# Optimization experiments

Hardware: AMD Instinct MI355X
Metric: run time of the kernel (lower is better)

The kernel has to match this reference:

```python
import jax, jax.numpy as jnp
import numpy as np

D_MODEL, D_STATE, D_CONV, EXPAND = 1024, 16, 4, 2
D_INNER = EXPAND * D_MODEL
B, L = 2, 2048


def setup_inputs() -> dict:
    key = jax.random.key(0)
    ks = jax.random.split(key, 8)
    s = lambda fan: 1.0 / np.sqrt(fan)
    x = jax.random.normal(ks[0], (B, L, D_MODEL), dtype=jnp.float32)
    W_in = jax.random.normal(ks[1], (2 * D_INNER, D_MODEL), dtype=jnp.float32) * s(D_MODEL)
    conv_w = jax.random.normal(ks[2], (D_INNER, 1, D_CONV), dtype=jnp.float32) * s(D_CONV)
    conv_b = jax.random.normal(ks[3], (D_INNER,), dtype=jnp.float32) * 0.01
    A_log = jnp.log(jnp.abs(jax.random.normal(ks[4], (D_INNER, D_STATE), dtype=jnp.float32)) + 1e-4)
    Dp = jnp.ones((D_INNER,), dtype=jnp.float32)
    W_dt = jax.random.normal(ks[5], (D_INNER, D_INNER), dtype=jnp.float32) * s(D_INNER)
    b_dt = jax.random.normal(ks[6], (D_INNER,), dtype=jnp.float32) * 0.01
    W_out = jax.random.normal(ks[7], (D_MODEL, D_INNER), dtype=jnp.float32) * s(D_INNER)
    return {"x": x, "W_in": W_in, "conv_w": conv_w, "conv_b": conv_b,
            "A_log": A_log, "Dp": Dp, "W_dt": W_dt, "b_dt": b_dt, "W_out": W_out}


def _mamba_fwd(x, W_in, conv_w, conv_b, A_log, Dp, W_dt, b_dt, W_out):
    Bsz, Ln, _ = x.shape
    xz = x @ W_in.T                                  # [B, L, 2*d_inner]
    x_proj, z = jnp.split(xz, 2, axis=-1)            # each [B, L, d_inner]
    # depthwise causal conv1d: left-pad d_conv-1 (matches torch pad + [:L] slice)
    xc = jnp.transpose(x_proj, (0, 2, 1))            # [B, C, L]
    xc = jax.lax.conv_general_dilated(
        xc, conv_w, window_strides=(1,), padding=[(D_CONV - 1, 0)],
        dimension_numbers=("NCH", "OIH", "NCH"), feature_group_count=D_INNER)
    xc = xc + conv_b[None, :, None]
    x_act = jax.nn.silu(jnp.transpose(xc, (0, 2, 1)))  # [B, L, d_inner]
    dt = jax.nn.softplus(x_act @ W_dt.T + b_dt)        # [B, L, d_inner]
    A = -jnp.exp(A_log)                                # [d_inner, d_state]

    def step(h, inp):
        xt, dt_t = inp                                 # [B, d_inner] each
        dA = jnp.exp(dt_t[:, :, None] * A[None])       # [B, d_inner, d_state]
        dB = (dt_t * xt)[:, :, None]                   # broadcast over states
        h = dA * h + dB
        y_t = h.sum(axis=-1) + Dp * xt                 # [B, d_inner]
        return h, y_t

    h0 = jnp.zeros((Bsz, D_INNER, D_STATE), dtype=x.dtype)
    xs = (jnp.transpose(x_act, (1, 0, 2)), jnp.transpose(dt, (1, 0, 2)))  # [L, B, d_inner]
    _, ys = jax.lax.scan(step, h0, xs)
    y_ssm = jnp.transpose(ys, (1, 0, 2))               # [B, L, d_inner]
    y_gated = y_ssm * jax.nn.silu(z)
    return y_gated @ W_out.T                           # [B, L, d_model]


def reference(x, W_in, conv_w, conv_b, A_log, Dp, W_dt, b_dt, W_out):
    return _mamba_fwd(x, W_in, conv_w, conv_b, A_log, Dp, W_dt, b_dt, W_out)
```

## Files before the change

### kernel.cpp

```cpp
#include <hip/hip_runtime.h>

#define DMODEL 1024
#define DSTATE 16
#define DCONV  4
#define DINNER 2048
#define BSZ    2
#define LSEQ   2048
#define MTOT   (BSZ * LSEQ)
#define NCH    64
#define LC     (LSEQ / NCH)
#define LOG2E  1.44269504088896f

typedef unsigned short u16;
typedef __attribute__((ext_vector_type(8))) short short8;
typedef __attribute__((ext_vector_type(8))) unsigned short u16x8;
typedef __attribute__((ext_vector_type(4))) float f32x4;

__device__ __forceinline__ float silu_f(float v) {
  return v * __builtin_amdgcn_rcpf(1.f + __builtin_amdgcn_exp2f(-v * LOG2E));
}

__device__ __forceinline__ u16 f2bf(float f) {
  unsigned int u = __float_as_uint(f);
  u += 0x7FFF + ((u >> 16) & 1);
  return (u16)(u >> 16);
}
__device__ __forceinline__ float bf2f(u16 b) { return __uint_as_float(((unsigned int)b) << 16); }

__device__ __forceinline__ void gload_lds16(const u16* g, u16* l) {
  __builtin_amdgcn_global_load_lds((const __attribute__((address_space(1))) unsigned int*)g,
                                   (__attribute__((address_space(3))) unsigned int*)l, 16, 0, 0);
}

__global__ __launch_bounds__(256)
void cast4(const float4* __restrict__ s0, ushort4* __restrict__ d0, int n0,
           const float4* __restrict__ s1, ushort4* __restrict__ d1, int n1,
           const float4* __restrict__ s2, ushort4* __restrict__ d2, int n2,
           const float4* __restrict__ s3, ushort4* __restrict__ d3, int n3) {
  int i = blockIdx.x * 256 + threadIdx.x;
  const float4* s; ushort4* d;
  if (i < n0)                { s = s0; d = d0; }
  else if ((i -= n0) < n1)   { s = s1; d = d1; }
  else if ((i -= n1) < n2)   { s = s2; d = d2; }
  else if ((i -= n2) < n3)   { s = s3; d = d3; }
  else return;
  float4 v = s[i];
  ushort4 o = { f2bf(v.x), f2bf(v.y), f2bf(v.z), f2bf(v.w) };
  d[i] = o;
}

template<int BN, int MODE, int OBF>
__global__ __launch_bounds__(512, 2)
void gemm8p(const u16* __restrict__ A, const u16* __restrict__ Bm,
            const float* __restrict__ bias, void* __restrict__ Cv,
            int M, int N, int K) {
  constexpr int BT  = BN / 32;
  constexpr int TJP = 2;
  constexpr int NPH = BT / TJP;
  constexpr int NBH = BN / 128;
  extern __shared__ __align__(16) u16 smem[];
  u16* As = smem;
  u16* Bs = smem + 2 * 256 * 64;

  const int tid  = threadIdx.x;
  const int lane = tid & 63;
  const int w    = tid >> 6;
  const int quad = lane >> 4;
  const int l16  = lane & 15;
  const int wm   = (w >> 1) * 64;
  const int wn   = (w & 1) * (BN / 2);

  const int nbn = N / BN, nbm = M >> 8;
  const int pid = blockIdx.x;
  const int npg = 4 * nbn;
  const int fm  = (pid / npg) * 4;
  const int gsz = (nbm - fm < 4) ? (nbm - fm) : 4;
  const int bm  = (fm + (pid % gsz)) << 8;
  const int bn  = ((pid % npg) / gsz) * BN;

  const int rseg = lane >> 3;
  const int cd8  = (((lane & 7) ^ rseg) << 3);
  const u16* gA = A  + (size_t)(bm + 16 * w + rseg) * K + cd8;
  const u16* gB = Bm + (size_t)(bn + 16 * w + rseg) * K + cd8;
  u16* lA = &As[(2 * w) << 9];
  u16* lB = &Bs[(2 * w) << 9];
  const int Kmask = K - 1;

  auto stA = [&](int slot, int h, int kt) {
    const size_t go = (size_t)h * 128 * K + ((kt << 6) & Kmask);
    gload_lds16(gA + go,         lA + slot * 16384 + h * 8192);
    gload_lds16(gA + go + 8 * K, lA + slot * 16384 + h * 8192 + 512);
  };
  auto stB = [&](int slot, int h, int kt) {
    const size_t go = (size_t)h * 128 * K + ((kt << 6) & Kmask);
    gload_lds16(gB + go,         lB + slot * (BN * 64) + h * 8192);
    gload_lds16(gB + go + 8 * K, lB + slot * (BN * 64) + h * 8192 + 512);
  };

  int aoff[4][2], boff[BT][2];
#pragma unroll
  for (int t = 0; t < 4; ++t) {
    const int ra = wm + 16 * t + l16;
#pragma unroll
    for (int ks = 0; ks < 2; ++ks)
      aoff[t][ks] = ra * 64 + (((quad + 4 * ks) ^ (ra & 7)) << 3);
  }
#pragma unroll
  for (int tj = 0; tj < BT; ++tj) {
    const int rb = wn + 16 * tj + l16;
#pragma unroll
    for (int ks = 0; ks < 2; ++ks)
      boff[tj][ks] = rb * 64 + (((quad + 4 * ks) ^ (rb & 7)) << 3);
  }

  f32x4 acc[4][BT] = {};
  short8 af[4][2];

#define RD_AF(slot)                                                          \
  { _Pragma("unroll") for (int t = 0; t < 4; ++t)                            \
      _Pragma("unroll") for (int ks = 0; ks < 2; ++ks)                       \
        af[t][ks] = *(const short8*)&As[(slot) * 16384 + aoff[t][ks]]; }

#define VM4 asm volatile("s_waitcnt vmcnt(4)" ::: "memory")
#define NOWAIT ((void)0)

#define PHASE(slot, j, STG, WAIT)                                            \
  {                                                                          \
    if ((j) == 0) RD_AF(slot);                                               \
    short8 bfp[TJP][2];                                                      \
    _Pragma("unroll") for (int jj = 0; jj < TJP; ++jj)                       \
      _Pragma("unroll") for (int ks = 0; ks < 2; ++ks)                       \
        bfp[jj][ks] = *(const short8*)&Bs[(slot) * (BN * 64) +               \
                                          boff[(j) * TJP + jj][ks]];         \
    STG;                                                                     \
    __builtin_amdgcn_s_setprio(1);                                           \
    _Pragma("unroll") for (int ks = 0; ks < 2; ++ks)                         \
      _Pragma("unroll") for (int jj = 0; jj < TJP; ++jj)                     \
        _Pragma("unroll") for (int t = 0; t < 4; ++t)                        \
          acc[t][(j) * TJP + jj] = __builtin_amdgcn_mfma_f32_16x16x32_bf16(  \
              af[t][ks], bfp[jj][ks], acc[t][(j) * TJP + jj], 0, 0, 0);      \
    __builtin_amdgcn_s_setprio(0);                                           \
    asm volatile("s_waitcnt lgkmcnt(0)" ::: "memory");                       \
    WAIT;                                                                    \
    __builtin_amdgcn_s_barrier();                                            \
  }

  stA(0, 0, 0); stA(0, 1, 0);
  stB(0, 0, 0); if (NBH == 2) stB(0, 1, 0);
  stA(1, 0, 1); stA(1, 1, 1);
  VM4;
  __builtin_amdgcn_s_barrier();

  const int niter = K >> 7;
  for (int i = 0; i < niter; ++i) {
    const int tb1 = 2 * i + 1, t2 = 2 * i + 2, t3 = 2 * i + 3;
    if constexpr (NPH == 4) {
      PHASE(0, 0, { stB(1, 0, tb1); },               NOWAIT);
      PHASE(0, 1, { stB(1, 1, tb1); stA(0, 0, t2); }, NOWAIT);
      PHASE(0, 2, { stA(0, 1, t2); },                NOWAIT);
      PHASE(0, 3, {},                                VM4);
      PHASE(1, 0, { stB(0, 0, t2); },                NOWAIT);
      PHASE(1, 1, { stB(0, 1, t2); stA(1, 0, t3); }, NOWAIT);
      PHASE(1, 2, { stA(1, 1, t3); },                NOWAIT);
      PHASE(1, 3, {},                                VM4);
    } else {
      PHASE(0, 0, { stB(1, 0, tb1); },                NOWAIT);
      PHASE(0, 1, { stA(0, 0, t2); stA(0, 1, t2); },  VM4);
      PHASE(1, 0, { stB(0, 0, t2); },                 NOWAIT);
      PHASE(1, 1, { stA(1, 0, t3); stA(1, 1, t3); },  VM4);
    }
  }
#undef PHASE
#undef RD_AF
#undef VM4
#undef NOWAIT

  asm volatile("s_waitcnt vmcnt(0)" ::: "memory");

#pragma unroll
  for (int t = 0; t < 4; ++t) {
    const int row0 = bm + wm + 16 * t + quad * 4;
#pragma unroll
    for (int tj = 0; tj < BT; ++tj) {
      const int col = bn + wn + 16 * tj + l16;
      const float bv = (MODE == 1) ? bias[col] : 0.f;
#pragma unroll
      for (int i2 = 0; i2 < 4; ++i2) {
        float v = acc[t][tj][i2] + bv;
        if (MODE == 1) v = (v > 20.f) ? v : __logf(1.f + __expf(v));
        if (OBF) ((u16*)Cv)[(size_t)(row0 + i2) * N + col] = f2bf(v);
        else     ((float*)Cv)[(size_t)(row0 + i2) * N + col] = v;
      }
    }
  }
}

template<int MODE, int OBF, int BN>
__global__ __launch_bounds__(256)
void hgemm_bk128(const u16* __restrict__ A, const u16* __restrict__ B,
                 const float* __restrict__ bias, void* __restrict__ Cv,
                 int M, int N, int K) {
  constexpr int ASEG = 32;
  constexpr int BSEG = BN / 4;
  constexpr int SPW  = (ASEG + BSEG) / 4;
  constexpr int BT   = BN / 32;
  __shared__ u16 As[128 * 128];
  __shared__ u16 Bs[BN * 128];
  const int tid  = threadIdx.x;
  const int lane = tid & 63;
  const int w    = tid >> 6;
  const int quad = lane >> 4;
  const int l16  = lane & 15;

  const int nbn = N / BN, nbm = M >> 7;
  const int pid = blockIdx.x;
  const int npg = 4 * nbn;
  const int fm  = (pid / npg) * 4;
  const int gsz = (nbm - fm < 4) ? (nbm - fm) : 4;
  const int bm  = (fm + (pid % gsz)) << 7;
  const int bn  = ((pid % npg) / gsz) * BN;

  const int wm = (w & 1) * 64;
  const int wn = (w >> 1) * (BN / 2);

  const int rs4 = lane >> 4;
  const u16* Gp[SPW]; u16* Lp[SPW];
#pragma unroll
  for (int q = 0; q < SPW; ++q) {
    const int g = w * SPW + q;
    if (g < ASEG) {
      const int r  = g * 4 + rs4;
      const int cdk = (lane & 15) ^ (r & 15);
      Gp[q] = A + (size_t)(bm + r) * K + (cdk << 3);
      Lp[q] = &As[g << 9];
    } else {
      const int r  = (g - ASEG) * 4 + rs4;
      const int cdk = (lane & 15) ^ (r & 15);
      Gp[q] = B + (size_t)(bn + r) * K + (cdk << 3);
      Lp[q] = &Bs[(g - ASEG) << 9];
    }
  }

  const short8* Afp[4][4];
  const short8* Bfp[BT][4];
#pragma unroll
  for (int t = 0; t < 4; ++t) {
    const int ra = wm + 16 * t + l16;
#pragma unroll
    for (int ks = 0; ks < 4; ++ks)
      Afp[t][ks] = (const short8*)&As[ra * 128 + (((quad + 4 * ks) ^ (ra & 15)) << 3)];
  }
#pragma unroll
  for (int t = 0; t < BT; ++t) {
    const int rb = wn + 16 * t + l16;
#pragma unroll
    for (int ks = 0; ks < 4; ++ks)
      Bfp[t][ks] = (const short8*)&Bs[rb * 128 + (((quad + 4 * ks) ^ (rb & 15)) << 3)];
  }

  f32x4 acc[4][BT] = {};

  for (int k0 = 0; k0 < K; k0 += 128) {
#pragma unroll
    for (int q = 0; q < SPW; ++q) { gload_lds16(Gp[q], Lp[q]); Gp[q] += 128; }
    __syncthreads();
#pragma unroll
    for (int ks = 0; ks < 4; ++ks) {
      short8 af[4], bf[BT];
#pragma unroll
      for (int t = 0; t < 4; ++t) af[t] = *Afp[t][ks];
#pragma unroll
      for (int t = 0; t < BT; ++t) bf[t] = *Bfp[t][ks];
#pragma unroll
      for (int ti = 0; ti < 4; ++ti)
#pragma unroll
        for (int tj = 0; tj < BT; ++tj)
          acc[ti][tj] = __builtin_amdgcn_mfma_f32_16x16x32_bf16(af[ti], bf[tj],
                                                                acc[ti][tj], 0, 0, 0);
    }
    __syncthreads();
  }

#pragma unroll
  for (int ti = 0; ti < 4; ++ti) {
    const int row0 = bm + wm + 16 * ti + quad * 4;
#pragma unroll
    for (int tj = 0; tj < BT; ++tj) {
      const int col = bn + wn + 16 * tj + l16;
      const float bv = (MODE == 1) ? bias[col] : 0.f;
#pragma unroll
      for (int i = 0; i < 4; ++i) {
        float v = acc[ti][tj][i] + bv;
        if (MODE == 1) v = (v > 20.f) ? v : __logf(1.f + __expf(v));
        if (OBF) ((u16*)Cv)[(size_t)(row0 + i) * N + col] = f2bf(v);
        else     ((float*)Cv)[(size_t)(row0 + i) * N + col] = v;
      }
    }
  }
}

__global__ __launch_bounds__(256)
void conv_silu(const u16* __restrict__ xz, const float* __restrict__ conv_w,
               const float* __restrict__ conv_b, u16* __restrict__ xact) {
  const int i = blockIdx.x * 256 + threadIdx.x;
  const int ko = i & 255;
  const int t  = (i >> 8) & (LSEQ - 1);
  const int b  = i >> 19;
  const int c  = ko << 3;
  float a[8];
  float4 w[8];
#pragma unroll
  for (int j = 0; j < 8; ++j) {
    a[j] = conv_b[c + j];
    w[j] = *(const float4*)(conv_w + (c + j) * DCONV);
  }
#pragma unroll
  for (int k = 0; k < DCONV; ++k) {
    const int tt = t + k - (DCONV - 1);
    if (tt >= 0) {
      const u16x8 v = *(const u16x8*)(xz + ((size_t)(b * LSEQ + tt) << 12) + c);
#pragma unroll
      for (int j = 0; j < 8; ++j)
        a[j] = fmaf(bf2f(v[j]), ((const float*)&w[j])[k], a[j]);
    }
  }
  u16x8 o;
#pragma unroll
  for (int j = 0; j < 8; ++j) o[j] = f2bf(silu_f(a[j]));
  *(u16x8*)(xact + ((size_t)(b * LSEQ + t) << 11) + c) = o;
}


__global__ __launch_bounds__(256, 2)
void scan_pass1(const u16* __restrict__ dtb, const u16* __restrict__ xact,
                const float* __restrict__ A_log,
                u16* __restrict__ hbuf, float* __restrict__ sumdt) {
  const int gid = blockIdx.x * 256 + threadIdx.x;
  const int c  = gid & (DINNER - 1);
  const int ch = (gid >> 11) & (NCH - 1);
  const int b  = gid >> 17;
  float a2[16];
#pragma unroll
  for (int s = 0; s < 16; ++s)
    a2[s] = -__expf(A_log[c * DSTATE + s]) * LOG2E;
  const size_t base = ((size_t)(b * LSEQ + ch * LC) << 11) + c;
  float h[16] = {};
  float sd = 0.f;
  for (int j = 0; j < LC; j += 2) {
    const float dt0 = bf2f(dtb [base + ((size_t)j << 11)]);
    const float xv0 = bf2f(xact[base + ((size_t)j << 11)]);
    const float dt1 = bf2f(dtb [base + ((size_t)(j + 1) << 11)]);
    const float xv1 = bf2f(xact[base + ((size_t)(j + 1) << 11)]);
    const float dx0 = dt0 * xv0, dx1 = dt1 * xv1;
    sd += dt0 + dt1;
#pragma unroll
    for (int s = 0; s < 16; ++s)
      h[s] = fmaf(__builtin_amdgcn_exp2f(dt0 * a2[s]), h[s], dx0);
#pragma unroll
    for (int s = 0; s < 16; ++s)
      h[s] = fmaf(__builtin_amdgcn_exp2f(dt1 * a2[s]), h[s], dx1);
  }
  u16x8* ho = (u16x8*)&hbuf[(((size_t)(b * NCH + ch) * DINNER) + c) << 4];
  u16x8 lo, hi;
#pragma unroll
  for (int s = 0; s < 8; ++s) { lo[s] = f2bf(h[s]); hi[s] = f2bf(h[8 + s]); }
  ho[0] = lo; ho[1] = hi;
  sumdt[(size_t)(b * NCH + ch) * DINNER + c] = sd;
}

__global__ __launch_bounds__(256)
void scan_combine(u16* __restrict__ hbuf, const float* __restrict__ sumdt,
                  const float* __restrict__ A_log) {
  const int gid = blockIdx.x * 256 + threadIdx.x;
  const int s = gid & 15;
  const int c = (gid >> 4) & (DINNER - 1);
  const int b = gid >> 15;
  const float a2 = -__expf(A_log[c * DSTATE + s]) * LOG2E;
  float h = 0.f;
  for (int k = 0; k < NCH; ++k) {
    const size_t o = (((size_t)(b * NCH + k) * DINNER) + c) * 16 + s;
    const float he = bf2f(hbuf[o]);
    const float sd = sumdt[(size_t)(b * NCH + k) * DINNER + c];
    hbuf[o] = f2bf(h);
    h = fmaf(__builtin_amdgcn_exp2f(sd * a2), h, he);
  }
}

__global__ __launch_bounds__(256, 2)
void scan_pass3(const u16* __restrict__ dtb, const u16* __restrict__ xact,
                const u16* __restrict__ xz, const float* __restrict__ A_log,
                const float* __restrict__ Dp, const u16* __restrict__ hbuf,
                u16* __restrict__ yg) {
  const int gid = blockIdx.x * 256 + threadIdx.x;
  const int c  = gid & (DINNER - 1);
  const int ch = (gid >> 11) & (NCH - 1);
  const int b  = gid >> 17;
  float a2[16];
#pragma unroll
  for (int s = 0; s < 16; ++s)
    a2[s] = -__expf(A_log[c * DSTATE + s]) * LOG2E;
  const float dp = Dp[c];
  float h[16];
  const u16x8* hi = (const u16x8*)&hbuf[(((size_t)(b * NCH + ch) * DINNER) + c) << 4];
  const u16x8 vlo = hi[0], vhi = hi[1];
#pragma unroll
  for (int s = 0; s < 8; ++s) { h[s] = bf2f(vlo[s]); h[8 + s] = bf2f(vhi[s]); }
  const size_t base  = ((size_t)(b * LSEQ + ch * LC) << 11) + c;
  const size_t zbase = ((size_t)(b * LSEQ + ch * LC) << 12) + DINNER + c;
  for (int j = 0; j < LC; j += 2) {
    const float dt0 = bf2f(dtb [base + ((size_t)j << 11)]);
    const float xv0 = bf2f(xact[base + ((size_t)j << 11)]);
    const float zv0 = bf2f(xz[zbase + ((size_t)j << 12)]);
    const float dt1 = bf2f(dtb [base + ((size_t)(j + 1) << 11)]);
    const float xv1 = bf2f(xact[base + ((size_t)(j + 1) << 11)]);
    const float zv1 = bf2f(xz[zbase + ((size_t)(j + 1) << 12)]);
    const float dx0 = dt0 * xv0, dx1 = dt1 * xv1;
    float y0 = 0.f, y1 = 0.f;
#pragma unroll
    for (int s = 0; s < 16; ++s) {
      h[s] = fmaf(__builtin_amdgcn_exp2f(dt0 * a2[s]), h[s], dx0);
      y0 += h[s];
    }
#pragma unroll
    for (int s = 0; s < 16; ++s) {
      h[s] = fmaf(__builtin_amdgcn_exp2f(dt1 * a2[s]), h[s], dx1);
      y1 += h[s];
    }
    y0 = fmaf(dp, xv0, y0);
    y1 = fmaf(dp, xv1, y1);
    yg[base + ((size_t)j << 11)]       = f2bf(y0 * silu_f(zv0));
    yg[base + ((size_t)(j + 1) << 11)] = f2bf(y1 * silu_f(zv1));
  }
}

extern "C" void kernel_launch(void* const* d_in, const int* in_sizes, int n_in,
                              void* d_out, int out_size, void* d_ws, size_t ws_size,
                              hipStream_t stream) {
  const float* x      = (const float*)d_in[0];
  const float* W_in   = (const float*)d_in[1];
  const float* conv_w = (const float*)d_in[2];
  const float* conv_b = (const float*)d_in[3];
  const float* A_log  = (const float*)d_in[4];
  const float* Dp     = (const float*)d_in[5];
  const float* W_dt   = (const float*)d_in[6];
  const float* b_dt   = (const float*)d_in[7];
  const float* W_out  = (const float*)d_in[8];
  float* out = (float*)d_out;

  u16* xz   = (u16*)d_ws;
  u16* dtb  = xz   + (size_t)MTOT * 2 * DINNER;
  u16* xbf  = dtb  + (size_t)MTOT * DINNER;
  u16* wibf = xbf  + (size_t)MTOT * DMODEL;
  u16* wdbf = wibf + (size_t)2 * DINNER * DMODEL;
  u16* wobf = wdbf + (size_t)DINNER * DINNER;
  u16* xact = wobf + (size_t)DMODEL * DINNER;
  u16* yg   = xact + (size_t)MTOT * DINNER;
  u16* hbuf = yg   + (size_t)MTOT * DINNER;
  float* sumdt = (float*)(hbuf + (size_t)BSZ * NCH * DINNER * 16);

  const dim3 blk(256);

  static bool s_attr = false;
  if (!s_attr) {
    hipFuncSetAttribute(reinterpret_cast<const void*>(&gemm8p<256, 0, 1>),
                        hipFuncAttributeMaxDynamicSharedMemorySize, 131072);
    hipFuncSetAttribute(reinterpret_cast<const void*>(&gemm8p<128, 1, 1>),
                        hipFuncAttributeMaxDynamicSharedMemorySize, 98304);
    s_attr = true;
  }

  const int n0 = MTOT * DMODEL / 4, n1 = 2 * DINNER * DMODEL / 4;
  const int n2 = DINNER * DINNER / 4, n3 = DMODEL * DINNER / 4;
  cast4<<<(n0 + n1 + n2 + n3) / 256, blk, 0, stream>>>(
      (const float4*)x, (ushort4*)xbf, n0,
      (const float4*)W_in, (ushort4*)wibf, n1,
      (const float4*)W_dt, (ushort4*)wdbf, n2,
      (const float4*)W_out, (ushort4*)wobf, n3);

  gemm8p<256, 0, 1><<<(MTOT / 256) * (2 * DINNER / 256), dim3(512), 131072, stream>>>(
      xbf, wibf, nullptr, xz, MTOT, 2 * DINNER, DMODEL);
  conv_silu<<<(MTOT * 256) / 256, blk, 0, stream>>>(xz, conv_w, conv_b, xact);
  gemm8p<128, 1, 1><<<(MTOT / 256) * (DINNER / 128), dim3(512), 98304, stream>>>(
      xact, wdbf, b_dt, dtb, MTOT, DINNER, DINNER);
  scan_pass1<<<BSZ * NCH * DINNER / 256, blk, 0, stream>>>(dtb, xact, A_log, hbuf, sumdt);
  scan_combine<<<BSZ * DINNER * 16 / 256, blk, 0, stream>>>(hbuf, sumdt, A_log);
  scan_pass3<<<BSZ * NCH * DINNER / 256, blk, 0, stream>>>(dtb, xact, xz, A_log, Dp, hbuf, yg);
  hgemm_bk128<0, 0, 64><<<(MTOT / 128) * (DMODEL / 64), blk, 0, stream>>>(
      yg, wobf, nullptr, out, MTOT, DMODEL, DINNER);
}
```

Before: 291.7 us.

## Route output projection through pipelined 8-wave GEMM and stage epilogue via LDS

Adds a BN=64 variant of the 8-wave, double-buffered, phase-pipelined gemm8p kernel, with a single-phase schedule and adjusted B-tile loading. The final output projection now uses it in place of the simpler hgemm_bk128 kernel. The gemm8p epilogue now writes accumulators into a swizzled LDS patch and then issues 16-byte row-contiguous global stores instead of scattered scalar stores. This targets poor pipelining in the last GEMM and uncoalesced epilogue stores for all gemm8p uses. In exchange it costs extra LDS traffic, a barrier, and fewer, larger blocks for the output GEMM.

```diff
diff --git a/kernel.cpp b/kernel.cpp
--- a/kernel.cpp
+++ b/kernel.cpp
@@ -80,10 +80,11 @@
 
   const int rseg = lane >> 3;
   const int cd8  = (((lane & 7) ^ rseg) << 3);
+  const int browB = (BN == 64) ? (8 * w) : (16 * w);
   const u16* gA = A  + (size_t)(bm + 16 * w + rseg) * K + cd8;
-  const u16* gB = Bm + (size_t)(bn + 16 * w + rseg) * K + cd8;
+  const u16* gB = Bm + (size_t)(bn + browB + rseg) * K + cd8;
   u16* lA = &As[(2 * w) << 9];
-  u16* lB = &Bs[(2 * w) << 9];
+  u16* lB = (BN == 64) ? &Bs[w << 9] : &Bs[(2 * w) << 9];
   const int Kmask = K - 1;
 
   auto stA = [&](int slot, int h, int kt) {
@@ -93,8 +94,12 @@
   };
   auto stB = [&](int slot, int h, int kt) {
     const size_t go = (size_t)h * 128 * K + ((kt << 6) & Kmask);
-    gload_lds16(gB + go,         lB + slot * (BN * 64) + h * 8192);
-    gload_lds16(gB + go + 8 * K, lB + slot * (BN * 64) + h * 8192 + 512);
+    if constexpr (BN == 64) {
+      gload_lds16(gB + go, lB + slot * (BN * 64));
+    } else {
+      gload_lds16(gB + go,         lB + slot * (BN * 64) + h * 8192);
+      gload_lds16(gB + go + 8 * K, lB + slot * (BN * 64) + h * 8192 + 512);
+    }
   };
 
   int aoff[4][2], boff[BT][2];
@@ -163,11 +168,14 @@
       PHASE(1, 1, { stB(0, 1, t2); stA(1, 0, t3); }, NOWAIT);
       PHASE(1, 2, { stA(1, 1, t3); },                NOWAIT);
       PHASE(1, 3, {},                                VM4);
-    } else {
+    } else if constexpr (NPH == 2) {
       PHASE(0, 0, { stB(1, 0, tb1); },                NOWAIT);
       PHASE(0, 1, { stA(0, 0, t2); stA(0, 1, t2); },  VM4);
       PHASE(1, 0, { stB(0, 0, t2); },                 NOWAIT);
       PHASE(1, 1, { stA(1, 0, t3); stA(1, 1, t3); },  VM4);
+    } else {
+      PHASE(0, 0, { stB(1, 0, tb1); stA(0, 0, t2); stA(0, 1, t2); }, VM4);
+      PHASE(1, 0, { stB(0, 0, t2);  stA(1, 0, t3); stA(1, 1, t3); }, VM4);
     }
   }
 #undef PHASE
@@ -176,125 +184,60 @@
 #undef NOWAIT
 
   asm volatile("s_waitcnt vmcnt(0)" ::: "memory");
-
-#pragma unroll
-  for (int t = 0; t < 4; ++t) {
-    const int row0 = bm + wm + 16 * t + quad * 4;
-#pragma unroll
-    for (int tj = 0; tj < BT; ++tj) {
-      const int col = bn + wn + 16 * tj + l16;
-      const float bv = (MODE == 1) ? bias[col] : 0.f;
-#pragma unroll
-      for (int i2 = 0; i2 < 4; ++i2) {
-        float v = acc[t][tj][i2] + bv;
-        if (MODE == 1) v = (v > 20.f) ? v : __logf(1.f + __expf(v));
-        if (OBF) ((u16*)Cv)[(size_t)(row0 + i2) * N + col] = f2bf(v);
-        else     ((float*)Cv)[(size_t)(row0 + i2) * N + col] = v;
+  __builtin_amdgcn_s_barrier();
+
+  constexpr int WTN = BN / 2;
+  if constexpr (OBF) {
+    constexpr int CPR = WTN / 8;
+    u16* patch = smem + (size_t)w * (64 * WTN);
+#pragma unroll
+    for (int t = 0; t < 4; ++t) {
+#pragma unroll
+      for (int tj = 0; tj < BT; ++tj) {
+        const int colb = 16 * tj + l16;
+        const float bv = (MODE == 1) ? bias[bn + wn + colb] : 0.f;
+#pragma unroll
+        for (int i2 = 0; i2 < 4; ++i2) {
+          const int row = 16 * t + quad * 4 + i2;
+          float v = acc[t][tj][i2] + bv;
+          if (MODE == 1) v = (v > 20.f) ? v : __logf(1.f + __expf(v));
+          patch[row * WTN + ((((colb >> 3) ^ (row & (CPR - 1))) << 3) | (colb & 7))] = f2bf(v);
+        }
       }
     }
-  }
-}
-
-template<int MODE, int OBF, int BN>
-__global__ __launch_bounds__(256)
-void hgemm_bk128(const u16* __restrict__ A, const u16* __restrict__ B,
-                 const float* __restrict__ bias, void* __restrict__ Cv,
-                 int M, int N, int K) {
-  constexpr int ASEG = 32;
-  constexpr int BSEG = BN / 4;
-  constexpr int SPW  = (ASEG + BSEG) / 4;
-  constexpr int BT   = BN / 32;
-  __shared__ u16 As[128 * 128];
-  __shared__ u16 Bs[BN * 128];
-  const int tid  = threadIdx.x;
-  const int lane = tid & 63;
-  const int w    = tid >> 6;
-  const int quad = lane >> 4;
-  const int l16  = lane & 15;
-
-  const int nbn = N / BN, nbm = M >> 7;
-  const int pid = blockIdx.x;
-  const int npg = 4 * nbn;
-  const int fm  = (pid / npg) * 4;
-  const int gsz = (nbm - fm < 4) ? (nbm - fm) : 4;
-  const int bm  = (fm + (pid % gsz)) << 7;
-  const int bn  = ((pid % npg) / gsz) * BN;
-
-  const int wm = (w & 1) * 64;
-  const int wn = (w >> 1) * (BN / 2);
-
-  const int rs4 = lane >> 4;
-  const u16* Gp[SPW]; u16* Lp[SPW];
-#pragma unroll
-  for (int q = 0; q < SPW; ++q) {
-    const int g = w * SPW + q;
-    if (g < ASEG) {
-      const int r  = g * 4 + rs4;
-      const int cdk = (lane & 15) ^ (r & 15);
-      Gp[q] = A + (size_t)(bm + r) * K + (cdk << 3);
-      Lp[q] = &As[g << 9];
-    } else {
-      const int r  = (g - ASEG) * 4 + rs4;
-      const int cdk = (lane & 15) ^ (r & 15);
-      Gp[q] = B + (size_t)(bn + r) * K + (cdk << 3);
-      Lp[q] = &Bs[(g - ASEG) << 9];
-    }
-  }
-
-  const short8* Afp[4][4];
-  const short8* Bfp[BT][4];
-#pragma unroll
-  for (int t = 0; t < 4; ++t) {
-    const int ra = wm + 16 * t + l16;
-#pragma unroll
-    for (int ks = 0; ks < 4; ++ks)
-      Afp[t][ks] = (const short8*)&As[ra * 128 + (((quad + 4 * ks) ^ (ra & 15)) << 3)];
-  }
-#pragma unroll
-  for (int t = 0; t < BT; ++t) {
-    const int rb = wn + 16 * t + l16;
-#pragma unroll
-    for (int ks = 0; ks < 4; ++ks)
-      Bfp[t][ks] = (const short8*)&Bs[rb * 128 + (((quad + 4 * ks) ^ (rb & 15)) << 3)];
-  }
-
-  f32x4 acc[4][BT] = {};
-
-  for (int k0 = 0; k0 < K; k0 += 128) {
-#pragma unroll
-    for (int q = 0; q < SPW; ++q) { gload_lds16(Gp[q], Lp[q]); Gp[q] += 128; }
-    __syncthreads();
-#pragma unroll
-    for (int ks = 0; ks < 4; ++ks) {
-      short8 af[4], bf[BT];
-#pragma unroll
-      for (int t = 0; t < 4; ++t) af[t] = *Afp[t][ks];
-#pragma unroll
-      for (int t = 0; t < BT; ++t) bf[t] = *Bfp[t][ks];
-#pragma unroll
-      for (int ti = 0; ti < 4; ++ti)
-#pragma unroll
-        for (int tj = 0; tj < BT; ++tj)
-          acc[ti][tj] = __builtin_amdgcn_mfma_f32_16x16x32_bf16(af[ti], bf[tj],
-                                                                acc[ti][tj], 0, 0, 0);
-    }
-    __syncthreads();
-  }
-
-#pragma unroll
-  for (int ti = 0; ti < 4; ++ti) {
-    const int row0 = bm + wm + 16 * ti + quad * 4;
-#pragma unroll
-    for (int tj = 0; tj < BT; ++tj) {
-      const int col = bn + wn + 16 * tj + l16;
-      const float bv = (MODE == 1) ? bias[col] : 0.f;
-#pragma unroll
-      for (int i = 0; i < 4; ++i) {
-        float v = acc[ti][tj][i] + bv;
-        if (MODE == 1) v = (v > 20.f) ? v : __logf(1.f + __expf(v));
-        if (OBF) ((u16*)Cv)[(size_t)(row0 + i) * N + col] = f2bf(v);
-        else     ((float*)Cv)[(size_t)(row0 + i) * N + col] = v;
+    asm volatile("s_waitcnt lgkmcnt(0)" ::: "memory");
+#pragma unroll
+    for (int it = 0; it < CPR; ++it) {
+      const int flat = it * 64 + lane;
+      const int row  = flat / CPR;
+      const int cc   = flat % CPR;
+      const u16x8 vv = *(const u16x8*)&patch[row * WTN + ((cc ^ (row & (CPR - 1))) << 3)];
+      *(u16x8*)((u16*)Cv + (size_t)(bm + wm + row) * N + bn + wn + cc * 8) = vv;
+    }
+  } else {
+    constexpr int CPR = WTN / 4;
+    float* patch = (float*)smem + (size_t)w * (64 * WTN);
+#pragma unroll
+    for (int t = 0; t < 4; ++t) {
+#pragma unroll
+      for (int tj = 0; tj < BT; ++tj) {
+        const int colb = 16 * tj + l16;
+#pragma unroll
+        for (int i2 = 0; i2 < 4; ++i2) {
+          const int row = 16 * t + quad * 4 + i2;
+          patch[row * WTN + ((((colb >> 2) ^ (row & (CPR - 1))) << 2) | (colb & 3))] =
+              acc[t][tj][i2];
+        }
       }
+    }
+    asm volatile("s_waitcnt lgkmcnt(0)" ::: "memory");
+#pragma unroll
+    for (int it = 0; it < CPR; ++it) {
+      const int flat = it * 64 + lane;
+      const int row  = flat / CPR;
+      const int cc   = flat % CPR;
+      const float4 vv = *(const float4*)&patch[row * WTN + ((cc ^ (row & (CPR - 1))) << 2)];
+      *(float4*)((float*)Cv + (size_t)(bm + wm + row) * N + bn + wn + cc * 4) = vv;
     }
   }
 }
@@ -466,6 +409,8 @@
                         hipFuncAttributeMaxDynamicSharedMemorySize, 131072);
     hipFuncSetAttribute(reinterpret_cast<const void*>(&gemm8p<128, 1, 1>),
                         hipFuncAttributeMaxDynamicSharedMemorySize, 98304);
+    hipFuncSetAttribute(reinterpret_cast<const void*>(&gemm8p<64, 0, 0>),
+                        hipFuncAttributeMaxDynamicSharedMemorySize, 81920);
     s_attr = true;
   }
 
@@ -485,6 +430,6 @@
   scan_pass1<<<BSZ * NCH * DINNER / 256, blk, 0, stream>>>(dtb, xact, A_log, hbuf, sumdt);
   scan_combine<<<BSZ * DINNER * 16 / 256, blk, 0, stream>>>(hbuf, sumdt, A_log);
   scan_pass3<<<BSZ * NCH * DINNER / 256, blk, 0, stream>>>(dtb, xact, xz, A_log, Dp, hbuf, yg);
-  hgemm_bk128<0, 0, 64><<<(MTOT / 128) * (DMODEL / 64), blk, 0, stream>>>(
+  gemm8p<64, 0, 0><<<(MTOT / 256) * (DMODEL / 64), dim3(512), 81920, stream>>>(
       yg, wobf, nullptr, out, MTOT, DMODEL, DINNER);
 }
```

After: 293.6 us. Within noise of the previous version (+0.6%).

## Fuse three scan stages into one cooperative kernel with grid syncs

Applied to the files above, without the earlier changes.

Merges scan_pass1, scan_combine and scan_pass3 into a single cooperative kernel that uses grid-wide syncs between stages, so two kernel launches and their inter-kernel gaps go away. The A_log-derived coefficients are computed once per thread and reused in both passes. It raises launch bounds to 4 blocks per CU so all 1024 blocks can be co-resident, which may limit registers. If the cooperative launch fails, the code falls back to the original three kernels.

```diff
diff --git a/kernel.cpp b/kernel.cpp
--- a/kernel.cpp
+++ b/kernel.cpp
@@ -1,4 +1,7 @@
 #include <hip/hip_runtime.h>
+#include <hip/hip_cooperative_groups.h>
+
+namespace cg = cooperative_groups;
 
 #define DMODEL 1024
 #define DSTATE 16
@@ -331,18 +334,10 @@
 }
 
 
-__global__ __launch_bounds__(256, 2)
-void scan_pass1(const u16* __restrict__ dtb, const u16* __restrict__ xact,
-                const float* __restrict__ A_log,
-                u16* __restrict__ hbuf, float* __restrict__ sumdt) {
-  const int gid = blockIdx.x * 256 + threadIdx.x;
-  const int c  = gid & (DINNER - 1);
-  const int ch = (gid >> 11) & (NCH - 1);
-  const int b  = gid >> 17;
-  float a2[16];
-#pragma unroll
-  for (int s = 0; s < 16; ++s)
-    a2[s] = -__expf(A_log[c * DSTATE + s]) * LOG2E;
+__device__ __forceinline__ void scan_p1_core(
+    int c, int ch, int b, const float* a2, const u16* __restrict__ dtb,
+    const u16* __restrict__ xact, u16* __restrict__ hbuf,
+    float* __restrict__ sumdt) {
   const size_t base = ((size_t)(b * LSEQ + ch * LC) << 11) + c;
   float h[16] = {};
   float sd = 0.f;
@@ -368,10 +363,9 @@
   sumdt[(size_t)(b * NCH + ch) * DINNER + c] = sd;
 }
 
-__global__ __launch_bounds__(256)
-void scan_combine(u16* __restrict__ hbuf, const float* __restrict__ sumdt,
-                  const float* __restrict__ A_log) {
-  const int gid = blockIdx.x * 256 + threadIdx.x;
+__device__ __forceinline__ void scan_comb_core(
+    int gid, u16* __restrict__ hbuf, const float* __restrict__ sumdt,
+    const float* __restrict__ A_log) {
   const int s = gid & 15;
   const int c = (gid >> 4) & (DINNER - 1);
   const int b = gid >> 15;
@@ -386,20 +380,11 @@
   }
 }
 
-__global__ __launch_bounds__(256, 2)
-void scan_pass3(const u16* __restrict__ dtb, const u16* __restrict__ xact,
-                const u16* __restrict__ xz, const float* __restrict__ A_log,
-                const float* __restrict__ Dp, const u16* __restrict__ hbuf,
-                u16* __restrict__ yg) {
-  const int gid = blockIdx.x * 256 + threadIdx.x;
-  const int c  = gid & (DINNER - 1);
-  const int ch = (gid >> 11) & (NCH - 1);
-  const int b  = gid >> 17;
-  float a2[16];
-#pragma unroll
-  for (int s = 0; s < 16; ++s)
-    a2[s] = -__expf(A_log[c * DSTATE + s]) * LOG2E;
-  const float dp = Dp[c];
+__device__ __forceinline__ void scan_p3_core(
+    int c, int ch, int b, const float* a2, float dp,
+    const u16* __restrict__ dtb, const u16* __restrict__ xact,
+    const u16* __restrict__ xz, const u16* __restrict__ hbuf,
+    u16* __restrict__ yg) {
   float h[16];
   const u16x8* hi = (const u16x8*)&hbuf[(((size_t)(b * NCH + ch) * DINNER) + c) << 4];
   const u16x8 vlo = hi[0], vhi = hi[1];
@@ -431,6 +416,68 @@
     yg[base + ((size_t)j << 11)]       = f2bf(y0 * silu_f(zv0));
     yg[base + ((size_t)(j + 1) << 11)] = f2bf(y1 * silu_f(zv1));
   }
+}
+
+__global__ __launch_bounds__(256, 4)
+void scan_fused(const u16* __restrict__ dtb, const u16* __restrict__ xact,
+                const u16* __restrict__ xz, const float* __restrict__ A_log,
+                const float* __restrict__ Dp, u16* __restrict__ hbuf,
+                float* __restrict__ sumdt, u16* __restrict__ yg) {
+  cg::grid_group grid = cg::this_grid();
+  const int gid = blockIdx.x * 256 + threadIdx.x;
+  const int c  = gid & (DINNER - 1);
+  const int ch = (gid >> 11) & (NCH - 1);
+  const int b  = gid >> 17;
+  float a2[16];
+#pragma unroll
+  for (int s = 0; s < 16; ++s)
+    a2[s] = -__expf(A_log[c * DSTATE + s]) * LOG2E;
+  const float dp = Dp[c];
+
+  scan_p1_core(c, ch, b, a2, dtb, xact, hbuf, sumdt);
+  grid.sync();
+  if (gid < BSZ * DINNER * DSTATE)
+    scan_comb_core(gid, hbuf, sumdt, A_log);
+  grid.sync();
+  scan_p3_core(c, ch, b, a2, dp, dtb, xact, xz, hbuf, yg);
+}
+
+__global__ __launch_bounds__(256, 2)
+void scan_pass1(const u16* __restrict__ dtb, const u16* __restrict__ xact,
+                const float* __restrict__ A_log,
+                u16* __restrict__ hbuf, float* __restrict__ sumdt) {
+  const int gid = blockIdx.x * 256 + threadIdx.x;
+  const int c  = gid & (DINNER - 1);
+  const int ch = (gid >> 11) & (NCH - 1);
+  const int b  = gid >> 17;
+  float a2[16];
+#pragma unroll
+  for (int s = 0; s < 16; ++s)
+    a2[s] = -__expf(A_log[c * DSTATE + s]) * LOG2E;
+  scan_p1_core(c, ch, b, a2, dtb, xact, hbuf, sumdt);
+}
+
+__global__ __launch_bounds__(256)
+void scan_combine(u16* __restrict__ hbuf, const float* __restrict__ sumdt,
+                  const float* __restrict__ A_log) {
+  const int gid = blockIdx.x * 256 + threadIdx.x;
+  scan_comb_core(gid, hbuf, sumdt, A_log);
+}
+
+__global__ __launch_bounds__(256, 2)
+void scan_pass3(const u16* __restrict__ dtb, const u16* __restrict__ xact,
+                const u16* __restrict__ xz, const float* __restrict__ A_log,
+                const float* __restrict__ Dp, const u16* __restrict__ hbuf,
+                u16* __restrict__ yg) {
+  const int gid = blockIdx.x * 256 + threadIdx.x;
+  const int c  = gid & (DINNER - 1);
+  const int ch = (gid >> 11) & (NCH - 1);
+  const int b  = gid >> 17;
+  float a2[16];
+#pragma unroll
+  for (int s = 0; s < 16; ++s)
+    a2[s] = -__expf(A_log[c * DSTATE + s]) * LOG2E;
+  scan_p3_core(c, ch, b, a2, Dp[c], dtb, xact, xz, hbuf, yg);
 }
 
 extern "C" void kernel_launch(void* const* d_in, const int* in_sizes, int n_in,
@@ -482,9 +529,23 @@
   conv_silu<<<(MTOT * 256) / 256, blk, 0, stream>>>(xz, conv_w, conv_b, xact);
   gemm8p<128, 1, 1><<<(MTOT / 256) * (DINNER / 128), dim3(512), 98304, stream>>>(
       xact, wdbf, b_dt, dtb, MTOT, DINNER, DINNER);
-  scan_pass1<<<BSZ * NCH * DINNER / 256, blk, 0, stream>>>(dtb, xact, A_log, hbuf, sumdt);
-  scan_combine<<<BSZ * DINNER * 16 / 256, blk, 0, stream>>>(hbuf, sumdt, A_log);
-  scan_pass3<<<BSZ * NCH * DINNER / 256, blk, 0, stream>>>(dtb, xact, xz, A_log, Dp, hbuf, yg);
+
+  {
+    const u16* dtb_c = dtb; const u16* xact_c = xact; const u16* xz_c = xz;
+    void* kargs[] = { (void*)&dtb_c, (void*)&xact_c, (void*)&xz_c,
+                      (void*)&A_log, (void*)&Dp, (void*)&hbuf,
+                      (void*)&sumdt, (void*)&yg };
+    hipError_t ce = hipLaunchCooperativeKernel(
+        reinterpret_cast<const void*>(&scan_fused),
+        dim3(BSZ * NCH * DINNER / 256), dim3(256), kargs, 0, stream);
+    if (ce != hipSuccess) {
+      (void)hipGetLastError();
+      scan_pass1<<<BSZ * NCH * DINNER / 256, blk, 0, stream>>>(dtb, xact, A_log, hbuf, sumdt);
+      scan_combine<<<BSZ * DINNER * 16 / 256, blk, 0, stream>>>(hbuf, sumdt, A_log);
+      scan_pass3<<<BSZ * NCH * DINNER / 256, blk, 0, stream>>>(dtb, xact, xz, A_log, Dp, hbuf, yg);
+    }
+  }
+
   hgemm_bk128<0, 0, 64><<<(MTOT / 128) * (DMODEL / 64), blk, 0, stream>>>(
       yg, wobf, nullptr, out, MTOT, DMODEL, DINNER);
 }
```

Measured after the change: 543.0 us. +86.1%, slower.
